# Performance work log

Measured on AMD Instinct MI355X. Metric: run time of the kernel, lower is better.

Reference implementation:

```python
import jax, jax.numpy as jnp
import numpy as np

N_NODES = 100000
N_EDGES = 1600000
D = 128          # in_channels // 4
IN_CH = 512
OUT_CH = 256
NUM_LABELS = 4


def setup_inputs() -> dict:
    key = jax.random.key(0)
    k1, k2, k3, k4, k5, k6 = jax.random.split(key, 6)
    x = jax.random.normal(k1, (N_NODES, D), dtype=jnp.float32)
    edge_index = jax.random.randint(k2, (2, N_EDGES), 0, N_NODES, dtype=jnp.int64)
    edge_label = jax.random.uniform(k3, (N_EDGES, NUM_LABELS), dtype=jnp.float32)
    # Parameters (uniform init per module's reset_parameters)
    stdv_w = 1.0 / np.sqrt(IN_CH)
    stdv_t = 1.0 / np.sqrt(NUM_LABELS)
    weight = jax.random.uniform(k4, (IN_CH, OUT_CH), minval=-stdv_w, maxval=stdv_w, dtype=jnp.float32)
    trans_weight = jax.random.uniform(k5, (NUM_LABELS, D), minval=-stdv_t, maxval=stdv_t, dtype=jnp.float32)
    bias = jax.random.uniform(k6, (OUT_CH,), minval=-stdv_w, maxval=stdv_w, dtype=jnp.float32)
    return {"x": x, "edge_index": edge_index, "edge_label": edge_label,
            "weight": weight, "trans_weight": trans_weight, "bias": bias}


def _scatter_mean(vals, idx, num_segments):
    # segment mean; empty segments -> 0 (matches torch_scatter.scatter_mean)
    s = jax.ops.segment_sum(vals, idx, num_segments=num_segments)
    cnt = jax.ops.segment_sum(jnp.ones((vals.shape[0],), dtype=vals.dtype), idx,
                              num_segments=num_segments)
    return s / jnp.maximum(cnt, 1.0)[:, None]


def reference(x, edge_index, edge_label, weight, trans_weight, bias):
    row, col = edge_index[0], edge_index[1]
    n = x.shape[0]
    # edge-label transform: [E, L] @ [L, D] -> [E, D]
    elt = jnp.matmul(edge_label, trans_weight)
    opinion = _scatter_mean(elt, row, n)        # outgoing opinion aggregation
    out = _scatter_mean(x[col], row, n)          # outgoing neighbor features
    inn_opinion = _scatter_mean(elt, col, n)     # incoming opinion aggregation
    inn = _scatter_mean(x[row], col, n)          # incoming neighbor features
    h = jnp.concatenate((out, opinion, inn, inn_opinion), axis=1)  # [N, 4D]
    return jnp.matmul(h, weight) + bias
```

## Files before the change

kernel.cpp:

```cpp
#include <hip/hip_runtime.h>
#include <hip/hip_bf16.h>


#define BK 128
#define CHUNK 4096
#define CPT 16
#define CAP 4096
#define LDA 296

typedef unsigned short u16;
typedef unsigned long long u64;
typedef __attribute__((ext_vector_type(4))) float f32x4;
typedef __attribute__((ext_vector_type(8))) short bf16x8;

__device__ inline unsigned pk_bf16(float a, float b) {
    __hip_bfloat162 h;
    h.x = __float2bfloat16(a);
    h.y = __float2bfloat16(b);
    return *reinterpret_cast<unsigned*>(&h);
}
__device__ inline float2 upk_bf16(unsigned u) {
    __hip_bfloat162 h = *reinterpret_cast<__hip_bfloat162*>(&u);
    return make_float2(__bfloat162float(h.x), __bfloat162float(h.y));
}
__device__ inline u16 f2bf(float f) {
    __hip_bfloat16 h = __float2bfloat16(f);
    return *reinterpret_cast<u16*>(&h);
}

__global__ __launch_bounds__(256) void cvt_hist(
    const float2* __restrict__ x2, unsigned* __restrict__ xh,
    const int* __restrict__ eidx,
    int* __restrict__ cnt_r, int* __restrict__ cnt_c, int n2, int E, int nbk)
{
    __shared__ int hr[1024], hc[1024];
    const int t = threadIdx.x;
    const int gsz = gridDim.x * 256;
    for (int i = blockIdx.x * 256 + t; i < n2; i += gsz) {
        const float2 v = x2[i];
        xh[i] = pk_bf16(v.x, v.y);
    }
    for (int i = t; i < nbk; i += 256) { hr[i] = 0; hc[i] = 0; }
    __syncthreads();
    for (int e = blockIdx.x * 256 + t; e < E; e += gsz) {
        atomicAdd(&hr[((unsigned)eidx[e]) >> 7], 1);
        atomicAdd(&hc[((unsigned)eidx[E + e]) >> 7], 1);
    }
    __syncthreads();
    for (int i = t; i < nbk; i += 256) {
        if (hr[i]) atomicAdd(&cnt_r[i], hr[i]);
        if (hc[i]) atomicAdd(&cnt_c[i], hc[i]);
    }
}

__global__ __launch_bounds__(256) void prep_wb2(const float* __restrict__ w,
                                                const float* __restrict__ tw,
                                                u16* __restrict__ wb)
{
    __shared__ float P[8][256];
    const int pid0 = blockIdx.x * 256;
    const int t = threadIdx.x;
    if (pid0 + 255 >= 8192) {
        for (int q = t; q < 2048; q += 256) {
            const int l = q >> 8;
            const int cidx = q & 255;
            const int lr = l & 3;
            const int off = (l < 4) ? 128 : 384;
            float s = 0.f;
            for (int c = 0; c < 128; ++c)
                s = fmaf(tw[lr * 128 + c], w[(size_t)(off + c) * 256 + cidx], s);
            P[l][cidx] = s;
        }
        __syncthreads();
    }
    const int pid = pid0 + t;
    if (pid >= 9 * 16 * 64) return;
    const int ks = pid >> 10;
    const int ct = (pid >> 6) & 15;
    const int l  = pid & 63;
    const int col = ct * 16 + (l & 15);
    const int k0 = ks * 32 + ((l >> 4) << 3);
    u16 v[8];
    #pragma unroll
    for (int j = 0; j < 8; ++j) {
        const int k = k0 + j;
        float f = 0.f;
        if (k < 128)      f = w[(size_t)k * 256 + col];
        else if (k < 256) f = w[(size_t)(k + 128) * 256 + col];
        else if (k < 264) f = P[k - 256][col];
        v[j] = f2bf(f);
    }
    *(uint4*)(wb + (size_t)pid * 8) = *(uint4*)v;
}

__global__ __launch_bounds__(1024) void scan_b(const int* __restrict__ cnt_r,
                                               const int* __restrict__ cnt_c,
                                               int* __restrict__ boff_r,
                                               int* __restrict__ boff_c,
                                               int* __restrict__ cur_r,
                                               int* __restrict__ cur_c, int nbk)
{
    __shared__ int sh[1024];
    const int t = threadIdx.x;
    const int* cnt = blockIdx.x ? cnt_c : cnt_r;
    int* boff = blockIdx.x ? boff_c : boff_r;
    int* cur  = blockIdx.x ? cur_c  : cur_r;
    const int v = (t < nbk) ? cnt[t] : 0;
    sh[t] = v;
    __syncthreads();
    for (int s = 1; s < 1024; s <<= 1) {
        const int tmp = (t >= s) ? sh[t - s] : 0;
        __syncthreads();
        sh[t] += tmp;
        __syncthreads();
    }
    if (t < nbk) { const int off = sh[t] - v; boff[t] = off; cur[t] = off; }
    if (t == 0) boff[nbk] = sh[1023];
}

__global__ __launch_bounds__(256) void bin8r(
    const int* __restrict__ eidx, const float4* __restrict__ elab4,
    int* __restrict__ cur_r, int* __restrict__ cur_c,
    uint2* __restrict__ ent_r, uint2* __restrict__ ent_c, int E, int nbk)
{
    __shared__ int cR[1024], cC[1024];
    unsigned er[CPT], ec[CPT], lq[CPT];
    const int t = threadIdx.x;
    const int base = blockIdx.x * CHUNK;
    for (int i = t; i < nbk; i += 256) { cR[i] = 0; cC[i] = 0; }
    __syncthreads();
    #pragma unroll
    for (int j = 0; j < CPT; ++j) {
        const int e = base + j * 256 + t;
        if (e < E) {
            const unsigned row = (unsigned)eidx[e];
            const unsigned col = (unsigned)eidx[E + e];
            er[j] = row; ec[j] = col;
            const float4 lb = elab4[e];
            const unsigned q0 = (unsigned)(lb.x * 255.f + 0.5f);
            const unsigned q1 = (unsigned)(lb.y * 255.f + 0.5f);
            const unsigned q2 = (unsigned)(lb.z * 255.f + 0.5f);
            const unsigned q3 = (unsigned)(lb.w * 255.f + 0.5f);
            lq[j] = q0 | (q1 << 8) | (q2 << 16) | (q3 << 24);
            atomicAdd(&cR[row >> 7], 1);
            atomicAdd(&cC[col >> 7], 1);
        } else {
            er[j] = 0xFFFFFFFFu;
        }
    }
    __syncthreads();
    for (int b = t; b < nbk; b += 256) {
        int c = cR[b]; cR[b] = c ? atomicAdd(&cur_r[b], c) : 0;
        c = cC[b];     cC[b] = c ? atomicAdd(&cur_c[b], c) : 0;
    }
    __syncthreads();
    #pragma unroll
    for (int j = 0; j < CPT; ++j) {
        const unsigned row = er[j];
        if (row != 0xFFFFFFFFu) {
            const unsigned col = ec[j];
            const unsigned lv = lq[j];
            const int p = atomicAdd(&cR[row >> 7], 1);
            ent_r[p] = make_uint2(col | ((row & 127u) << 17), lv);
            const int q = atomicAdd(&cC[col >> 7], 1);
            ent_c[q] = make_uint2(row | ((col & 127u) << 17), lv);
        }
    }
}

__device__ inline void addrow(float* acc, const uint4 r) {
    const float2 a = upk_bf16(r.x), b = upk_bf16(r.y),
                 c = upk_bf16(r.z), d = upk_bf16(r.w);
    acc[0] += a.x; acc[1] += a.y; acc[2] += b.x; acc[3] += b.y;
    acc[4] += c.x; acc[5] += c.y; acc[6] += d.x; acc[7] += d.y;
}

__global__ __launch_bounds__(256) void sort_accum(
    const uint2* __restrict__ ent1_r, const uint2* __restrict__ ent1_c,
    const int* __restrict__ boff_r, const int* __restrict__ boff_c,
    const uint4* __restrict__ xh4,
    uint4* __restrict__ om4, uint4* __restrict__ im4,
    u16* __restrict__ labr_h, u16* __restrict__ labc_h, int nn, int nbk)
{
    __shared__ unsigned sorted[CAP];
    __shared__ int hist[BK], sc[BK], curs[BK];
    __shared__ u64 labacc[BK];
    const int t = threadIdx.x;
    const int dir = (blockIdx.x >= (unsigned)nbk);
    const int b = blockIdx.x - (dir ? nbk : 0);
    const uint2* __restrict__ buf1 = dir ? ent1_c : ent1_r;
    const int* __restrict__ boff = dir ? boff_c : boff_r;
    uint4* __restrict__ mean4 = dir ? im4 : om4;
    u16* __restrict__ labh = dir ? labc_h : labr_h;
    const int s0 = boff[b];
    int cnt = boff[b + 1] - s0;
    if (cnt > CAP) cnt = CAP;

    if (t < BK) { hist[t] = 0; labacc[t] = 0ull; }
    __syncthreads();
    for (int i = t; i < cnt; i += 256) {
        const uint2 en = buf1[s0 + i];
        const unsigned local = en.x >> 17;
        atomicAdd(&hist[local], 1);
        const unsigned lv = en.y;
        const u64 spread = (u64)(lv & 255u) | ((u64)((lv >> 8) & 255u) << 16)
                         | ((u64)((lv >> 16) & 255u) << 32) | ((u64)(lv >> 24) << 48);
        atomicAdd(&labacc[local], spread);
    }
    __syncthreads();
    if (t < BK) sc[t] = hist[t];
    __syncthreads();
    for (int s = 1; s < BK; s <<= 1) {
        int v = 0;
        if (t < BK && t >= s) v = sc[t - s];
        __syncthreads();
        if (t < BK) sc[t] += v;
        __syncthreads();
    }
    if (t < BK) {
        curs[t] = sc[t] - hist[t];
        const int gn = b * BK + t;
        if (gn < nn) {
            const u64 sv = labacc[t];
            const float inv = (1.f / 255.f) / fmaxf((float)hist[t], 1.f);
            u16 lm[4];
            #pragma unroll
            for (int l = 0; l < 4; ++l)
                lm[l] = f2bf((float)((sv >> (16 * l)) & 0xFFFFu) * inv);
            *(uint2*)(labh + (size_t)gn * 4) = *(uint2*)lm;
        }
    }
    __syncthreads();
    for (int i = t; i < cnt; i += 256) {
        const uint2 en = buf1[s0 + i];
        const int p = atomicAdd(&curs[en.x >> 17], 1);
        sorted[p] = en.x & 0x1FFFFu;
    }
    __syncthreads();

    const int wid = t >> 6;
    const int lane = t & 63;
    const int g = lane >> 4;
    const int sl = lane & 15;
    for (int local = wid; local < BK; local += 4) {
        const int gn = b * BK + local;
        if (gn >= nn) continue;
        const int segC = hist[local];
        const int segS = sc[local] - segC;
        float acc[8] = {0.f, 0.f, 0.f, 0.f, 0.f, 0.f, 0.f, 0.f};
        int i = 0;
        for (; i + 7 < segC; i += 8) {
            const unsigned p0 = sorted[segS + i + g];
            const unsigned p1 = sorted[segS + i + 4 + g];
            const uint4 r0 = xh4[(size_t)p0 * 16 + sl];
            const uint4 r1 = xh4[(size_t)p1 * 16 + sl];
            addrow(acc, r0);
            addrow(acc, r1);
        }
        if (i + 3 < segC) {
            const unsigned p0 = sorted[segS + i + g];
            const uint4 r0 = xh4[(size_t)p0 * 16 + sl];
            addrow(acc, r0);
            i += 4;
        }
        if (i + g < segC) {
            const unsigned p0 = sorted[segS + i + g];
            const uint4 r0 = xh4[(size_t)p0 * 16 + sl];
            addrow(acc, r0);
        }
        #pragma unroll
        for (int j = 0; j < 8; ++j) {
            acc[j] += __shfl_xor(acc[j], 16);
            acc[j] += __shfl_xor(acc[j], 32);
        }
        if (g == 0) {
            const float inv = 1.0f / fmaxf((float)segC, 1.0f);
            uint4 o;
            o.x = pk_bf16(acc[0] * inv, acc[1] * inv);
            o.y = pk_bf16(acc[2] * inv, acc[3] * inv);
            o.z = pk_bf16(acc[4] * inv, acc[5] * inv);
            o.w = pk_bf16(acc[6] * inv, acc[7] * inv);
            mean4[(size_t)gn * 16 + sl] = o;
        }
    }
}

__global__ __launch_bounds__(256) void gemm_mfma(
    const u16* __restrict__ om_h, const u16* __restrict__ im_h,
    const u16* __restrict__ labr_h, const u16* __restrict__ labc_h,
    const u16* __restrict__ wb, const float* __restrict__ bias,
    float* __restrict__ out, int nn)
{
    __shared__ u16 hA[64 * LDA];
    const int t = threadIdx.x;
    const int w = t >> 6;
    const int lane = t & 63;
    const int node0 = blockIdx.x * 64;

    for (int idx = t; idx < 2304; idx += 256) {
        const int row = idx / 36;
        const int c8 = idx - row * 36;
        const int gn = node0 + row;
        uint4 val = make_uint4(0, 0, 0, 0);
        if (gn < nn) {
            if (c8 < 16)
                val = *(const uint4*)(om_h + (size_t)gn * 128 + c8 * 8);
            else if (c8 < 32)
                val = *(const uint4*)(im_h + (size_t)gn * 128 + (c8 - 16) * 8);
            else if (c8 == 32) {
                const uint2 a = *(const uint2*)(labr_h + (size_t)gn * 4);
                const uint2 b = *(const uint2*)(labc_h + (size_t)gn * 4);
                val = make_uint4(a.x, a.y, b.x, b.y);
            }
        }
        *(uint4*)(&hA[row * LDA + c8 * 8]) = val;
    }
    __syncthreads();

    f32x4 acc[4][4];
    #pragma unroll
    for (int i = 0; i < 4; ++i)
        #pragma unroll
        for (int j = 0; j < 4; ++j)
            acc[i][j] = (f32x4){0.f, 0.f, 0.f, 0.f};

    const int m15 = lane & 15;
    const int kq  = lane >> 4;

    for (int ks = 0; ks < 9; ++ks) {
        const int koff = ks * 32 + kq * 8;
        bf16x8 af[4], bfr[4];
        #pragma unroll
        for (int nt = 0; nt < 4; ++nt)
            af[nt] = *(const bf16x8*)(&hA[(nt * 16 + m15) * LDA + koff]);
        #pragma unroll
        for (int c2 = 0; c2 < 4; ++c2)
            bfr[c2] = *(const bf16x8*)(wb + ((size_t)((ks * 16 + w * 4 + c2) * 64 + lane)) * 8);
        #pragma unroll
        for (int nt = 0; nt < 4; ++nt)
            #pragma unroll
            for (int c2 = 0; c2 < 4; ++c2)
                acc[nt][c2] = __builtin_amdgcn_mfma_f32_16x16x32_bf16(
                    af[nt], bfr[c2], acc[nt][c2], 0, 0, 0);
    }

    #pragma unroll
    for (int nt = 0; nt < 4; ++nt) {
        const int gnb = node0 + nt * 16 + kq * 4;
        #pragma unroll
        for (int c2 = 0; c2 < 4; ++c2) {
            const int oc = w * 64 + c2 * 16 + m15;
            const float bv = bias[oc];
            #pragma unroll
            for (int r = 0; r < 4; ++r) {
                const int gn = gnb + r;
                if (gn < nn) out[(size_t)gn * 256 + oc] = acc[nt][c2][r] + bv;
            }
        }
    }
}

extern "C" void kernel_launch(void* const* d_in, const int* in_sizes, int n_in,
                              void* d_out, int out_size, void* d_ws, size_t ws_size,
                              hipStream_t stream) {
    const float* x      = (const float*)d_in[0];
    const int*   eidx   = (const int*)d_in[1];
    const float* elabel = (const float*)d_in[2];
    const float* weight = (const float*)d_in[3];
    const float* tw     = (const float*)d_in[4];
    const float* bias   = (const float*)d_in[5];

    const int n = in_sizes[0] / 128;
    const int E = in_sizes[2] / 4;
    const int nbk = (n + BK - 1) / BK;

    char* wsb = (char*)d_ws;
    u16* om_h    = (u16*)wsb;   wsb += (size_t)n * 256;
    u16* im_h    = (u16*)wsb;   wsb += (size_t)n * 256;
    u16* labr_h  = (u16*)wsb;   wsb += (size_t)n * 8;
    u16* labc_h  = (u16*)wsb;   wsb += (size_t)n * 8;
    u16* wb      = (u16*)wsb;   wsb += 9216 * 16;
    int* cnt_r   = (int*)wsb;   wsb += nbk * 4;
    int* cnt_c   = (int*)wsb;   wsb += nbk * 4;
    int* boff_r  = (int*)wsb;   wsb += (nbk + 1) * 4;
    int* boff_c  = (int*)wsb;   wsb += (nbk + 1) * 4;
    int* cur_r   = (int*)wsb;   wsb += nbk * 4;
    int* cur_c   = (int*)wsb;   wsb += nbk * 4;

    unsigned* xh = (unsigned*)d_out;
    uint2* ent1_r = (uint2*)(xh + (size_t)n * 64);
    uint2* ent1_c = ent1_r + E;

    hipMemsetAsync(cnt_r, 0, (size_t)2 * nbk * sizeof(int), stream);

    hipLaunchKernelGGL(cvt_hist, dim3(512), dim3(256), 0, stream,
                       (const float2*)x, xh, eidx, cnt_r, cnt_c, n * 64, E, nbk);

    hipLaunchKernelGGL(prep_wb2, dim3(36), dim3(256), 0, stream, weight, tw, wb);

    hipLaunchKernelGGL(scan_b, dim3(2), dim3(1024), 0, stream,
                       cnt_r, cnt_c, boff_r, boff_c, cur_r, cur_c, nbk);

    hipLaunchKernelGGL(bin8r, dim3((E + CHUNK - 1) / CHUNK), dim3(256), 0, stream,
                       eidx, (const float4*)elabel, cur_r, cur_c, ent1_r, ent1_c, E, nbk);

    hipLaunchKernelGGL(sort_accum, dim3(2 * nbk), dim3(256), 0, stream,
                       ent1_r, ent1_c, boff_r, boff_c, (const uint4*)xh,
                       (uint4*)om_h, (uint4*)im_h, labr_h, labc_h, n, nbk);

    hipLaunchKernelGGL(gemm_mfma, dim3((n + 63) / 64), dim3(256), 0, stream,
                       om_h, im_h, labr_h, labc_h, wb, bias, (float*)d_out, n);
}
```

Measured before the change: 295.7 us.

## Merge weight prep into histogram kernel and split binning by direction

The weight-packing kernel is folded into the conversion/histogram kernel as extra blocks, which saves one launch and lets the two jobs overlap. The binning kernel now runs separate blocks for the row and column directions. Each block uses a single shared histogram and loads indices four at a time with int4 loads, so the grid doubles and per-block shared memory and register pressure drop. In exchange, the edge labels are read and quantized twice (once per direction), and the int4 loads assume E is a multiple of 4 and suitably aligned.

Result: faster. 278.7 us (-5.7%).

```diff
diff --git a/kernel.cpp b/kernel.cpp
--- a/kernel.cpp
+++ b/kernel.cpp
@@ -4,9 +4,9 @@
 
 #define BK 128
 #define CHUNK 4096
-#define CPT 16
 #define CAP 4096
 #define LDA 296
+#define NB_CVT 512
 
 typedef unsigned short u16;
 typedef unsigned long long u64;
@@ -28,14 +28,54 @@
     return *reinterpret_cast<u16*>(&h);
 }
 
-__global__ __launch_bounds__(256) void cvt_hist(
+__global__ __launch_bounds__(256) void cvt_hist_wb(
     const float2* __restrict__ x2, unsigned* __restrict__ xh,
     const int* __restrict__ eidx,
-    int* __restrict__ cnt_r, int* __restrict__ cnt_c, int n2, int E, int nbk)
+    int* __restrict__ cnt_r, int* __restrict__ cnt_c,
+    const float* __restrict__ w, const float* __restrict__ tw,
+    u16* __restrict__ wb, int n2, int E, int nbk)
 {
     __shared__ int hr[1024], hc[1024];
+    __shared__ float P[8][256];
     const int t = threadIdx.x;
-    const int gsz = gridDim.x * 256;
+
+    if (blockIdx.x >= NB_CVT) {
+        const int pid0 = (blockIdx.x - NB_CVT) * 256;
+        if (pid0 + 255 >= 8192) {
+            for (int q = t; q < 2048; q += 256) {
+                const int l = q >> 8;
+                const int cidx = q & 255;
+                const int lr = l & 3;
+                const int off = (l < 4) ? 128 : 384;
+                float s = 0.f;
+                for (int c = 0; c < 128; ++c)
+                    s = fmaf(tw[lr * 128 + c], w[(size_t)(off + c) * 256 + cidx], s);
+                P[l][cidx] = s;
+            }
+            __syncthreads();
+        }
+        const int pid = pid0 + t;
+        if (pid >= 9 * 16 * 64) return;
+        const int ks = pid >> 10;
+        const int ct = (pid >> 6) & 15;
+        const int l  = pid & 63;
+        const int col = ct * 16 + (l & 15);
+        const int k0 = ks * 32 + ((l >> 4) << 3);
+        u16 v[8];
+        #pragma unroll
+        for (int j = 0; j < 8; ++j) {
+            const int k = k0 + j;
+            float f = 0.f;
+            if (k < 128)      f = w[(size_t)k * 256 + col];
+            else if (k < 256) f = w[(size_t)(k + 128) * 256 + col];
+            else if (k < 264) f = P[k - 256][col];
+            v[j] = f2bf(f);
+        }
+        *(uint4*)(wb + (size_t)pid * 8) = *(uint4*)v;
+        return;
+    }
+
+    const int gsz = NB_CVT * 256;
     for (int i = blockIdx.x * 256 + t; i < n2; i += gsz) {
         const float2 v = x2[i];
         xh[i] = pk_bf16(v.x, v.y);
@@ -51,46 +91,6 @@
         if (hr[i]) atomicAdd(&cnt_r[i], hr[i]);
         if (hc[i]) atomicAdd(&cnt_c[i], hc[i]);
     }
-}
-
-__global__ __launch_bounds__(256) void prep_wb2(const float* __restrict__ w,
-                                                const float* __restrict__ tw,
-                                                u16* __restrict__ wb)
-{
-    __shared__ float P[8][256];
-    const int pid0 = blockIdx.x * 256;
-    const int t = threadIdx.x;
-    if (pid0 + 255 >= 8192) {
-        for (int q = t; q < 2048; q += 256) {
-            const int l = q >> 8;
-            const int cidx = q & 255;
-            const int lr = l & 3;
-            const int off = (l < 4) ? 128 : 384;
-            float s = 0.f;
-            for (int c = 0; c < 128; ++c)
-                s = fmaf(tw[lr * 128 + c], w[(size_t)(off + c) * 256 + cidx], s);
-            P[l][cidx] = s;
-        }
-        __syncthreads();
-    }
-    const int pid = pid0 + t;
-    if (pid >= 9 * 16 * 64) return;
-    const int ks = pid >> 10;
-    const int ct = (pid >> 6) & 15;
-    const int l  = pid & 63;
-    const int col = ct * 16 + (l & 15);
-    const int k0 = ks * 32 + ((l >> 4) << 3);
-    u16 v[8];
-    #pragma unroll
-    for (int j = 0; j < 8; ++j) {
-        const int k = k0 + j;
-        float f = 0.f;
-        if (k < 128)      f = w[(size_t)k * 256 + col];
-        else if (k < 256) f = w[(size_t)(k + 128) * 256 + col];
-        else if (k < 264) f = P[k - 256][col];
-        v[j] = f2bf(f);
-    }
-    *(uint4*)(wb + (size_t)pid * 8) = *(uint4*)v;
 }
 
 __global__ __launch_bounds__(1024) void scan_b(const int* __restrict__ cnt_r,
@@ -118,52 +118,67 @@
     if (t == 0) boff[nbk] = sh[1023];
 }
 
-__global__ __launch_bounds__(256) void bin8r(
+__global__ __launch_bounds__(256) void bin8r_dir(
     const int* __restrict__ eidx, const float4* __restrict__ elab4,
     int* __restrict__ cur_r, int* __restrict__ cur_c,
-    uint2* __restrict__ ent_r, uint2* __restrict__ ent_c, int E, int nbk)
+    uint2* __restrict__ ent_r, uint2* __restrict__ ent_c,
+    int E, int nbk, int nchunk)
 {
-    __shared__ int cR[1024], cC[1024];
-    unsigned er[CPT], ec[CPT], lq[CPT];
+    __shared__ int cB[1024];
     const int t = threadIdx.x;
-    const int base = blockIdx.x * CHUNK;
-    for (int i = t; i < nbk; i += 256) { cR[i] = 0; cC[i] = 0; }
-    __syncthreads();
+    const int dir = (blockIdx.x >= (unsigned)nchunk);
+    const int base = (dir ? blockIdx.x - nchunk : blockIdx.x) * CHUNK;
+    const int* __restrict__ osrc = eidx + (dir ? (size_t)E : 0);
+    const int* __restrict__ psrc = eidx + (dir ? 0 : (size_t)E);
+    int* __restrict__ cur = dir ? cur_c : cur_r;
+    uint2* __restrict__ ent = dir ? ent_c : ent_r;
+
+    for (int i = t; i < nbk; i += 256) cB[i] = 0;
+    __syncthreads();
+
+    int4 own4[4], par4[4];
+    unsigned lq[16];
+    bool ok[4];
     #pragma unroll
-    for (int j = 0; j < CPT; ++j) {
-        const int e = base + j * 256 + t;
-        if (e < E) {
-            const unsigned row = (unsigned)eidx[e];
-            const unsigned col = (unsigned)eidx[E + e];
-            er[j] = row; ec[j] = col;
-            const float4 lb = elab4[e];
-            const unsigned q0 = (unsigned)(lb.x * 255.f + 0.5f);
-            const unsigned q1 = (unsigned)(lb.y * 255.f + 0.5f);
-            const unsigned q2 = (unsigned)(lb.z * 255.f + 0.5f);
-            const unsigned q3 = (unsigned)(lb.w * 255.f + 0.5f);
-            lq[j] = q0 | (q1 << 8) | (q2 << 16) | (q3 << 24);
-            atomicAdd(&cR[row >> 7], 1);
-            atomicAdd(&cC[col >> 7], 1);
-        } else {
-            er[j] = 0xFFFFFFFFu;
+    for (int jj = 0; jj < 4; ++jj) {
+        const int e0 = base + (jj * 256 + t) * 4;
+        ok[jj] = (e0 < E);
+        if (ok[jj]) {
+            own4[jj] = *(const int4*)(osrc + e0);
+            par4[jj] = *(const int4*)(psrc + e0);
+            #pragma unroll
+            for (int k = 0; k < 4; ++k) {
+                const float4 lb = elab4[e0 + k];
+                const unsigned q0 = (unsigned)(lb.x * 255.f + 0.5f);
+                const unsigned q1 = (unsigned)(lb.y * 255.f + 0.5f);
+                const unsigned q2 = (unsigned)(lb.z * 255.f + 0.5f);
+                const unsigned q3 = (unsigned)(lb.w * 255.f + 0.5f);
+                lq[jj * 4 + k] = q0 | (q1 << 8) | (q2 << 16) | (q3 << 24);
+            }
+            atomicAdd(&cB[((unsigned)own4[jj].x) >> 7], 1);
+            atomicAdd(&cB[((unsigned)own4[jj].y) >> 7], 1);
+            atomicAdd(&cB[((unsigned)own4[jj].z) >> 7], 1);
+            atomicAdd(&cB[((unsigned)own4[jj].w) >> 7], 1);
         }
     }
     __syncthreads();
     for (int b = t; b < nbk; b += 256) {
-        int c = cR[b]; cR[b] = c ? atomicAdd(&cur_r[b], c) : 0;
-        c = cC[b];     cC[b] = c ? atomicAdd(&cur_c[b], c) : 0;
+        const int c = cB[b];
+        cB[b] = c ? atomicAdd(&cur[b], c) : 0;
     }
     __syncthreads();
     #pragma unroll
-    for (int j = 0; j < CPT; ++j) {
-        const unsigned row = er[j];
-        if (row != 0xFFFFFFFFu) {
-            const unsigned col = ec[j];
-            const unsigned lv = lq[j];
-            const int p = atomicAdd(&cR[row >> 7], 1);
-            ent_r[p] = make_uint2(col | ((row & 127u) << 17), lv);
-            const int q = atomicAdd(&cC[col >> 7], 1);
-            ent_c[q] = make_uint2(row | ((col & 127u) << 17), lv);
+    for (int jj = 0; jj < 4; ++jj) {
+        if (ok[jj]) {
+            const int owns[4] = {own4[jj].x, own4[jj].y, own4[jj].z, own4[jj].w};
+            const int pars[4] = {par4[jj].x, par4[jj].y, par4[jj].z, par4[jj].w};
+            #pragma unroll
+            for (int k = 0; k < 4; ++k) {
+                const unsigned own = (unsigned)owns[k];
+                const int p = atomicAdd(&cB[own >> 7], 1);
+                ent[p] = make_uint2((unsigned)pars[k] | ((own & 127u) << 17),
+                                    lq[jj * 4 + k]);
+            }
         }
     }
 }
@@ -373,6 +388,7 @@
     const int n = in_sizes[0] / 128;
     const int E = in_sizes[2] / 4;
     const int nbk = (n + BK - 1) / BK;
+    const int nchunk = (E + CHUNK - 1) / CHUNK;
 
     char* wsb = (char*)d_ws;
     u16* om_h    = (u16*)wsb;   wsb += (size_t)n * 256;
@@ -393,16 +409,16 @@
 
     hipMemsetAsync(cnt_r, 0, (size_t)2 * nbk * sizeof(int), stream);
 
-    hipLaunchKernelGGL(cvt_hist, dim3(512), dim3(256), 0, stream,
-                       (const float2*)x, xh, eidx, cnt_r, cnt_c, n * 64, E, nbk);
-
-    hipLaunchKernelGGL(prep_wb2, dim3(36), dim3(256), 0, stream, weight, tw, wb);
+    hipLaunchKernelGGL(cvt_hist_wb, dim3(NB_CVT + 36), dim3(256), 0, stream,
+                       (const float2*)x, xh, eidx, cnt_r, cnt_c,
+                       weight, tw, wb, n * 64, E, nbk);
 
     hipLaunchKernelGGL(scan_b, dim3(2), dim3(1024), 0, stream,
                        cnt_r, cnt_c, boff_r, boff_c, cur_r, cur_c, nbk);
 
-    hipLaunchKernelGGL(bin8r, dim3((E + CHUNK - 1) / CHUNK), dim3(256), 0, stream,
-                       eidx, (const float4*)elabel, cur_r, cur_c, ent1_r, ent1_c, E, nbk);
+    hipLaunchKernelGGL(bin8r_dir, dim3(2 * nchunk), dim3(256), 0, stream,
+                       eidx, (const float4*)elabel, cur_r, cur_c,
+                       ent1_r, ent1_c, E, nbk, nchunk);
 
     hipLaunchKernelGGL(sort_accum, dim3(2 * nbk), dim3(256), 0, stream,
                        ent1_r, ent1_c, boff_r, boff_c, (const uint4*)xh,
```
